# Performance work log

Measured on AMD Instinct MI355X. Metric: run time of the kernel, lower is better.

The kernel has to match this reference:

```python
import jax, jax.numpy as jnp
import numpy as np

N_GRAMS = 3
N_KERNELS = 11

def _kernel_mus(K):
    l = [1.0]
    if K == 1:
        return l
    bs = 2.0 / (K - 1)
    l.append(1.0 - bs / 2.0)
    for i in range(1, K - 1):
        l.append(l[i] - bs)
    return l

def _kernel_sigmas(K):
    if K == 1:
        return [0.001]
    bs = 2.0 / (K - 1)
    return [0.001] + [0.5 * bs] * (K - 1)

MU = jnp.asarray(_kernel_mus(N_KERNELS), jnp.float32)       # (K,)
SIGMA = jnp.asarray(_kernel_sigmas(N_KERNELS), jnp.float32)  # (K,)

def _conv_relu(x, w, b):
    # x: (B,E,L), w: (O,E,h); right-pad h-1 so output length == L (as ConstantPad1d((0,h-1)))
    h = w.shape[-1]
    y = jax.lax.conv_general_dilated(x, w, (1,), [(0, h - 1)], dimension_numbers=('NCH', 'OIH', 'NCH'))
    return jax.nn.relu(y + b[None, :, None]).transpose(0, 2, 1)  # (B,L,O)

def _cosine(a, b):
    # CosineMatrixAttention: normalize rows then matmul
    an = a / (jnp.linalg.norm(a, axis=-1, keepdims=True) + 1e-13)
    bn = b / (jnp.linalg.norm(b, axis=-1, keepdims=True) + 1e-13)
    return jnp.einsum('bqe,bde->bqd', an, bn)

def setup_inputs() -> dict:
    key = jax.random.key(0)
    ks = jax.random.split(key, 12)
    B, Lq, Ld, V, E, O = 128, 64, 512, 30000, 300, 128
    inp = {}
    inp['tokens_q'] = jax.random.randint(ks[0], (B, Lq), 0, V)
    inp['tokens_d'] = jax.random.randint(ks[1], (B, Ld), 0, V)
    inp['emb'] = jax.random.normal(ks[2], (V, E), jnp.float32) * 0.1
    for i, h in enumerate((1, 2, 3)):
        inp['conv_w%d' % h] = jax.random.normal(ks[3 + i], (O, E, h), jnp.float32) * (1.0 / np.sqrt(E * h))
        inp['conv_b%d' % h] = jnp.zeros((O,), jnp.float32)
    inp['fc_w'] = jax.random.normal(ks[9], (1, N_KERNELS * N_GRAMS * N_GRAMS), jnp.float32) * 0.1
    inp['fc_b'] = jnp.zeros((1,), jnp.float32)
    return inp

def reference(tokens_q, tokens_d, emb, conv_w1, conv_b1, conv_w2, conv_b2, conv_w3, conv_b3, fc_w, fc_b):
    qmask = (tokens_q > 0).astype(jnp.float32)  # (B,Lq)
    dmask = (tokens_d > 0).astype(jnp.float32)  # (B,Ld)
    qe = emb[tokens_q].transpose(0, 2, 1)  # (B,E,Lq)
    de = emb[tokens_d].transpose(0, 2, 1)  # (B,E,Ld)
    cws = [(conv_w1, conv_b1), (conv_w2, conv_b2), (conv_w3, conv_b3)]
    hq = [_conv_relu(qe, w, b) for w, b in cws]  # each (B,Lq,O)
    hd = [_conv_relu(de, w, b) for w, b in cws]  # each (B,Ld,O)
    pair_mask = qmask[:, :, None] * dmask[:, None, :]  # (B,Lq,Ld)
    mu = MU[None, None, None, :]
    sig = SIGMA[None, None, None, :]
    feats = []
    for q in range(N_GRAMS):
        for d in range(N_GRAMS):
            m = _cosine(hq[q], hd[d]) * pair_mask  # (B,Lq,Ld)
            rbf = jnp.exp(-jnp.square(m[..., None] - mu) / (2.0 * jnp.square(sig))) * pair_mask[..., None]
            qk = rbf.sum(axis=2)  # (B,Lq,K)
            logk = jnp.log(jnp.maximum(qk, 1e-10)) * 0.01
            # NOTE: original has a typo (loq_ vs log_) so the query mask is NOT applied before summing
            feats.append(logk.sum(axis=1))  # (B,K)
    cross = jnp.concatenate(feats, axis=-1)  # (B, K*G*G)
    return cross @ fc_w.T + fc_b  # (B,1)
```

## Files before the change

### kernel.cpp

```cpp
#include <hip/hip_runtime.h>
#include <hip/hip_bf16.h>

typedef __attribute__((ext_vector_type(8))) short short8;
typedef __attribute__((ext_vector_type(4))) float f32x4;

#define E_DIM 300
#define NCH   128
#define NOUT  384
#define NCHUNK 30

__device__ __forceinline__ unsigned short f2bf(float f) {
    unsigned int u = __float_as_uint(f);
    u += 0x7FFFu + ((u >> 16) & 1u);
    return (unsigned short)(u >> 16);
}
__device__ __forceinline__ float bf2f(unsigned short s) {
    return __uint_as_float(((unsigned int)s) << 16);
}

__global__ void pack_wb(const float* __restrict__ w1, const float* __restrict__ w2,
                        const float* __restrict__ w3, unsigned short* __restrict__ Wp) {
    int idx = blockIdx.x * 256 + threadIdx.x;
    if (idx >= NCHUNK * NOUT * 32) return;
    int ke = idx & 31;
    int n  = (idx >> 5) % NOUT;
    int c  = idx / (32 * NOUT);
    int s  = c / 10;
    int e  = (c % 10) * 32 + ke;
    int g  = n >> 7, o = n & 127, h = g + 1;
    float v = 0.0f;
    if (e < E_DIM && s < h) {
        const float* w = (g == 0) ? w1 : ((g == 1) ? w2 : w3);
        v = w[(o * E_DIM + e) * h + s];
    }
    Wp[idx] = f2bf(v);
}

__launch_bounds__(256, 3)
__global__ void conv_mfma(const int* __restrict__ tokens_q, const int* __restrict__ tokens_d,
                          const float* __restrict__ emb, const unsigned short* __restrict__ Wp,
                          const float* __restrict__ b1, const float* __restrict__ b2,
                          const float* __restrict__ b3,
                          unsigned short* __restrict__ hq, unsigned short* __restrict__ hd) {
    __shared__ __align__(16) short xs[66 * 320];
    __shared__ float bias_s[NOUT];
    __shared__ float nrm[64 * 3];
    __shared__ int   toks_s[66];

    int bx   = blockIdx.x;
    int b    = bx / 9;
    int tile = bx % 9;
    int isq  = (tile == 0);
    int L    = isq ? 64 : 512;
    int t0   = isq ? 0 : (tile - 1) * 64;
    const int* toks = isq ? (tokens_q + b * 64) : (tokens_d + b * 512);
    int tid  = threadIdx.x;
    int lane = tid & 63;
    int wn   = tid >> 6;
    int lr   = lane & 15;
    int lg   = lane >> 4;

    const unsigned short* wp0 = Wp + (size_t)(wn * 96 + lr) * 32 + lg * 8;
    short8 bbc[6], bbn[6];
    #pragma unroll
    for (int j = 0; j < 6; ++j) bbc[j] = *(const short8*)(wp0 + j * 512);

    if (tid < 66) toks_s[tid] = (t0 + tid < L) ? toks[t0 + tid] : -1;
    for (int i = tid; i < NOUT; i += 256) {
        int g = i >> 7, o = i & 127;
        bias_s[i] = (g == 0 ? b1 : (g == 1 ? b2 : b3))[o];
    }
    if (tid < 192) nrm[tid] = 0.0f;
    {
        uint4 z = {0, 0, 0, 0};
        uint4* xz = (uint4*)xs;
        for (int i = tid; i < 2640; i += 256) xz[i] = z;
    }
    __syncthreads();

    for (int i = tid; i < 66 * 75; i += 256) {
        int r = i / 75, f4 = i - r * 75;
        int tk = toks_s[r];
        if (tk >= 0) {
            float4 v = *(const float4*)(emb + (size_t)tk * E_DIM + f4 * 4);
            ushort4 u;
            u.x = f2bf(v.x); u.y = f2bf(v.y); u.z = f2bf(v.z); u.w = f2bf(v.w);
            int byte = (f4 * 8) ^ ((r & 7) << 4);
            *(ushort4*)((char*)xs + r * 640 + byte) = u;
        }
    }
    __syncthreads();

    f32x4 acc[4][6];
    #pragma unroll
    for (int i = 0; i < 4; ++i)
        #pragma unroll
        for (int j = 0; j < 6; ++j) acc[i][j] = (f32x4){0.f, 0.f, 0.f, 0.f};

    #pragma unroll 2
    for (int c = 0; c < NCHUNK; ++c) {
        if (c < NCHUNK - 1) {
            const unsigned short* wp = wp0 + (size_t)(c + 1) * NOUT * 32;
            #pragma unroll
            for (int j = 0; j < 6; ++j) bbn[j] = *(const short8*)(wp + j * 512);
        }
        int s  = c / 10;
        int ec = c - s * 10;
        short8 a[4];
        #pragma unroll
        for (int i = 0; i < 4; ++i) {
            int row  = i * 16 + lr + s;
            int byte = (ec * 64 + lg * 16) ^ ((row & 7) << 4);
            a[i] = *(const short8*)((const char*)xs + row * 640 + byte);
        }
        #pragma unroll
        for (int i = 0; i < 4; ++i)
            #pragma unroll
            for (int j = 0; j < 6; ++j)
                acc[i][j] = __builtin_amdgcn_mfma_f32_16x16x32_bf16(a[i], bbc[j], acc[i][j], 0, 0, 0);
        #pragma unroll
        for (int j = 0; j < 6; ++j) bbc[j] = bbn[j];
    }

    #pragma unroll
    for (int j = 0; j < 6; ++j) {
        float bv = bias_s[wn * 96 + j * 16 + lr];
        #pragma unroll
        for (int i = 0; i < 4; ++i)
            #pragma unroll
            for (int r = 0; r < 4; ++r) {
                float v = acc[i][j][r] + bv;
                acc[i][j][r] = v > 0.0f ? v : 0.0f;
            }
    }

    int  gfirst = (wn * 96) >> 7;
    bool spans  = ((wn * 96) & 127) + 96 > 128;

    float sqA[4][4], sqB[4][4];
    #pragma unroll
    for (int i = 0; i < 4; ++i)
        #pragma unroll
        for (int r = 0; r < 4; ++r) { sqA[i][r] = 0.0f; sqB[i][r] = 0.0f; }
    #pragma unroll
    for (int j = 0; j < 6; ++j) {
        int t = ((wn * 96 + j * 16) >> 7) - gfirst;
        #pragma unroll
        for (int i = 0; i < 4; ++i)
            #pragma unroll
            for (int r = 0; r < 4; ++r) {
                float v = acc[i][j][r] * acc[i][j][r];
                if (t == 0) sqA[i][r] += v; else sqB[i][r] += v;
            }
    }
    #pragma unroll
    for (int i = 0; i < 4; ++i)
        #pragma unroll
        for (int r = 0; r < 4; ++r) {
            float v = sqA[i][r];
            v += __shfl_xor(v, 1, 16);
            v += __shfl_xor(v, 2, 16);
            v += __shfl_xor(v, 4, 16);
            v += __shfl_xor(v, 8, 16);
            sqA[i][r] = v;
            float w = sqB[i][r];
            w += __shfl_xor(w, 1, 16);
            w += __shfl_xor(w, 2, 16);
            w += __shfl_xor(w, 4, 16);
            w += __shfl_xor(w, 8, 16);
            sqB[i][r] = w;
        }
    if (lr == 0) {
        #pragma unroll
        for (int i = 0; i < 4; ++i)
            #pragma unroll
            for (int r = 0; r < 4; ++r) {
                int row = i * 16 + lg * 4 + r;
                atomicAdd(&nrm[row * 3 + gfirst], sqA[i][r]);
                if (spans) atomicAdd(&nrm[row * 3 + gfirst + 1], sqB[i][r]);
            }
    }
    __syncthreads();

    float invA[4][4], invB[4][4];
    #pragma unroll
    for (int i = 0; i < 4; ++i)
        #pragma unroll
        for (int r = 0; r < 4; ++r) {
            int row = i * 16 + lg * 4 + r;
            invA[i][r] = 1.0f / (sqrtf(nrm[row * 3 + gfirst]) + 1e-13f);
            invB[i][r] = spans ? 1.0f / (sqrtf(nrm[row * 3 + gfirst + 1]) + 1e-13f) : 0.0f;
        }

    unsigned short* outp = isq ? hq : hd;
    #pragma unroll
    for (int j = 0; j < 6; ++j) {
        int n = wn * 96 + j * 16 + lr;
        int g = n >> 7, o = n & 127;
        int t = g - gfirst;
        #pragma unroll
        for (int i = 0; i < 4; ++i)
            #pragma unroll
            for (int r = 0; r < 4; ++r) {
                int row = i * 16 + lg * 4 + r;
                float inv = t ? invB[i][r] : invA[i][r];
                outp[((size_t)(g * 128 + b) * L + t0 + row) * NCH + o] = f2bf(acc[i][j][r] * inv);
            }
    }
}

#define QPITCH 136
__launch_bounds__(256, 3)
__global__ void sim_rbf(const unsigned short* __restrict__ hq,
                        const unsigned short* __restrict__ hd,
                        const int* __restrict__ tokens_q, const int* __restrict__ tokens_d,
                        float* __restrict__ cross) {
    __shared__ __align__(16) short qs[64 * QPITCH];
    __shared__ __align__(16) short ds2[2][64 * QPITCH];
    __shared__ unsigned char dm_s[512];
    __shared__ float logk_s[11];

    int bx = blockIdx.x;
    int b  = bx / 9;
    int p  = bx % 9;
    int gq = p / 3;
    int gd = p % 3;
    int tid = threadIdx.x;
    int lane = tid & 63;
    int wn   = tid >> 6;
    int lr   = lane & 15;
    int lg   = lane >> 4;

    if (tid < 11) logk_s[tid] = 0.0f;
    for (int i = tid; i < 512; i += 256)
        dm_s[i] = (tokens_d[b * 512 + i] > 0) ? 1 : 0;

    const unsigned short* qsrc = hq + ((size_t)(gq * 128 + b) * 64) * NCH;
    const unsigned short* dsrc = hd + ((size_t)(gd * 128 + b) * 512) * NCH;

    #pragma unroll
    for (int it = 0; it < 4; ++it) {
        int row  = it * 16 + (tid >> 4);
        int col8 = (tid & 15) * 8;
        *(uint4*)&qs[row * QPITCH + col8] = *(const uint4*)&qsrc[row * NCH + col8];
    }
    #pragma unroll
    for (int it = 0; it < 4; ++it) {
        int row  = it * 16 + (tid >> 4);
        int col8 = (tid & 15) * 8;
        *(uint4*)&ds2[0][row * QPITCH + col8] = *(const uint4*)&dsrc[row * NCH + col8];
    }
    __syncthreads();

    int q  = wn * 16 + lr;
    float qm = (tokens_q[b * 64 + q] > 0) ? 1.0f : 0.0f;

    short8 qf[4];
    #pragma unroll
    for (int ks = 0; ks < 4; ++ks)
        qf[ks] = *(const short8*)&qs[(wn * 16 + lr) * QPITCH + ks * 32 + lg * 8];

    float qk[11];
    #pragma unroll
    for (int k = 0; k < 11; ++k) qk[k] = 0.0f;

    const float C4 = 0.0183156389f;

    for (int ch = 0; ch < 8; ++ch) {
        int buf = ch & 1;
        uint4 r4[4];
        if (ch < 7) {
            #pragma unroll
            for (int it = 0; it < 4; ++it) {
                int row  = it * 16 + (tid >> 4);
                int col8 = (tid & 15) * 8;
                r4[it] = *(const uint4*)&dsrc[((size_t)(ch + 1) * 64 + row) * NCH + col8];
            }
        }

        #pragma unroll
        for (int mt = 0; mt < 4; ++mt) {
            f32x4 acc = (f32x4){0.f, 0.f, 0.f, 0.f};
            #pragma unroll
            for (int ks = 0; ks < 4; ++ks) {
                short8 a = *(const short8*)&ds2[buf][(mt * 16 + lr) * QPITCH + ks * 32 + lg * 8];
                acc = __builtin_amdgcn_mfma_f32_16x16x32_bf16(a, qf[ks], acc, 0, 0, 0);
            }
            uchar4 du = *(const uchar4*)&dm_s[ch * 64 + mt * 16 + lg * 4];
            float cv[4], cm[4];
            cm[0] = qm * (float)du.x; cm[1] = qm * (float)du.y;
            cm[2] = qm * (float)du.z; cm[3] = qm * (float)du.w;
            #pragma unroll
            for (int r = 0; r < 4; ++r) cv[r] = acc[r] * cm[r];

            float cmx = fmaxf(fmaxf(cv[0], cv[1]), fmaxf(cv[2], cv[3]));
            if (__any(cmx > 0.98f)) {
                #pragma unroll
                for (int r = 0; r < 4; ++r) {
                    if (cv[r] > 0.98f) {
                        float t0 = cv[r] - 1.0f;
                        qk[0] += __expf(-500000.0f * t0 * t0);
                    }
                }
            }
            #pragma unroll
            for (int r = 0; r < 4; ++r) {
                float c  = cv[r];
                float tA = c - 0.1f;
                float TA = __expf(-50.0f * tA * tA) * cm[r];
                float UA = __expf(20.0f * c - 4.0f);
                float tB = c + 0.1f;
                float TB = __expf(-50.0f * tB * tB) * cm[r];
                float UB = __expf(-20.0f * c - 4.0f);
                qk[5] += TA;
                TA *= UA; qk[4] += TA; UA *= C4;
                TA *= UA; qk[3] += TA; UA *= C4;
                TA *= UA; qk[2] += TA; UA *= C4;
                TA *= UA; qk[1] += TA;
                qk[6] += TB;
                TB *= UB; qk[7] += TB; UB *= C4;
                TB *= UB; qk[8] += TB; UB *= C4;
                TB *= UB; qk[9] += TB; UB *= C4;
                TB *= UB; qk[10] += TB;
            }
        }

        if (ch < 7) {
            #pragma unroll
            for (int it = 0; it < 4; ++it) {
                int row  = it * 16 + (tid >> 4);
                int col8 = (tid & 15) * 8;
                *(uint4*)&ds2[buf ^ 1][row * QPITCH + col8] = r4[it];
            }
        }
        __syncthreads();
    }

    #pragma unroll
    for (int k = 0; k < 11; ++k) {
        float v = qk[k];
        v += __shfl_xor(v, 16);
        v += __shfl_xor(v, 32);
        qk[k] = v;
    }
    if (lg == 0) {
        #pragma unroll
        for (int k = 0; k < 11; ++k) {
            float lv = __logf(fmaxf(qk[k], 1e-10f)) * 0.01f;
            atomicAdd(&logk_s[k], lv);
        }
    }
    __syncthreads();
    if (tid < 11) cross[b * 99 + p * 11 + tid] = logk_s[tid];
}

__global__ void fc_kernel(const float* __restrict__ cross, const float* __restrict__ fc_w,
                          const float* __restrict__ fc_b, float* __restrict__ out) {
    int b = threadIdx.x;
    float acc = fc_b[0];
    #pragma unroll 11
    for (int j = 0; j < 99; ++j) acc += cross[b * 99 + j] * fc_w[j];
    out[b] = acc;
}

extern "C" void kernel_launch(void* const* d_in, const int* in_sizes, int n_in,
                              void* d_out, int out_size, void* d_ws, size_t ws_size,
                              hipStream_t stream) {
    const int*   tq  = (const int*)d_in[0];
    const int*   td  = (const int*)d_in[1];
    const float* emb = (const float*)d_in[2];
    const float* w1  = (const float*)d_in[3];
    const float* cb1 = (const float*)d_in[4];
    const float* w2  = (const float*)d_in[5];
    const float* cb2 = (const float*)d_in[6];
    const float* w3  = (const float*)d_in[7];
    const float* cb3 = (const float*)d_in[8];
    const float* fcw = (const float*)d_in[9];
    const float* fcb = (const float*)d_in[10];

    char* ws = (char*)d_ws;
    unsigned short* Wp    = (unsigned short*)ws;
    float*          cross = (float*)(ws + 921600);
    unsigned short* hq    = (unsigned short*)(ws + 1048576);
    unsigned short* hd    = (unsigned short*)(ws + 8388608);

    hipLaunchKernelGGL(pack_wb, dim3(1440), dim3(256), 0, stream, w1, w2, w3, Wp);
    hipLaunchKernelGGL(conv_mfma, dim3(128 * 9), dim3(256), 0, stream,
                       tq, td, emb, Wp, cb1, cb2, cb3, hq, hd);
    hipLaunchKernelGGL(sim_rbf, dim3(128 * 9), dim3(256), 0, stream, hq, hd, tq, td, cross);
    hipLaunchKernelGGL(fc_kernel, dim3(1), dim3(128), 0, stream, cross, fcw, fcb, (float*)d_out);
}
```

Baseline: 194.0 us.

## Restructure conv kernel to 512 threads with per-group warps and shift-aware MFMA skipping

The conv kernel now runs 8 waves per block. Each wave owns 16 output channels across all three n-gram groups, replacing the earlier scheme of 96 contiguous packed columns per wave. The 30-chunk loop is split into three shift phases, and phase S only issues MFMAs for groups g>=S, so it skips the zero-padded weight chunks of the h=1 and h=2 convolutions (about a third of the MFMAs). The embedding gather is merged with zero-fill into a single pass, and the norm reduction is simplified now that each wave's columns sit inside known groups. The trade-offs are more atomics per row, higher register pressure under launch_bounds(512,4), and fewer accumulators per wave.

```diff
diff --git a/kernel.cpp b/kernel.cpp
--- a/kernel.cpp
+++ b/kernel.cpp
@@ -36,16 +36,14 @@
     Wp[idx] = f2bf(v);
 }
 
-__launch_bounds__(256, 3)
+__launch_bounds__(512, 4)
 __global__ void conv_mfma(const int* __restrict__ tokens_q, const int* __restrict__ tokens_d,
                           const float* __restrict__ emb, const unsigned short* __restrict__ Wp,
                           const float* __restrict__ b1, const float* __restrict__ b2,
                           const float* __restrict__ b3,
                           unsigned short* __restrict__ hq, unsigned short* __restrict__ hd) {
     __shared__ __align__(16) short xs[66 * 320];
-    __shared__ float bias_s[NOUT];
     __shared__ float nrm[64 * 3];
-    __shared__ int   toks_s[66];
 
     int bx   = blockIdx.x;
     int b    = bx / 9;
@@ -60,151 +58,88 @@
     int lr   = lane & 15;
     int lg   = lane >> 4;
 
-    const unsigned short* wp0 = Wp + (size_t)(wn * 96 + lr) * 32 + lg * 8;
-    short8 bbc[6], bbn[6];
-    #pragma unroll
-    for (int j = 0; j < 6; ++j) bbc[j] = *(const short8*)(wp0 + j * 512);
-
-    if (tid < 66) toks_s[tid] = (t0 + tid < L) ? toks[t0 + tid] : -1;
-    for (int i = tid; i < NOUT; i += 256) {
-        int g = i >> 7, o = i & 127;
-        bias_s[i] = (g == 0 ? b1 : (g == 1 ? b2 : b3))[o];
-    }
     if (tid < 192) nrm[tid] = 0.0f;
-    {
-        uint4 z = {0, 0, 0, 0};
-        uint4* xz = (uint4*)xs;
-        for (int i = tid; i < 2640; i += 256) xz[i] = z;
+
+    for (int i = tid; i < 66 * 80; i += 512) {
+        int r   = i / 80;
+        int f4  = i - r * 80;
+        int byt = (f4 * 8) ^ ((r & 7) << 4);
+        ushort4 u = {0, 0, 0, 0};
+        int pos = t0 + r;
+        if (f4 < 75 && pos < L) {
+            int tk = toks[pos];
+            float4 v = *(const float4*)(emb + (size_t)tk * E_DIM + f4 * 4);
+            u.x = f2bf(v.x); u.y = f2bf(v.y); u.z = f2bf(v.z); u.w = f2bf(v.w);
+        }
+        *(ushort4*)((char*)xs + r * 640 + byt) = u;
     }
     __syncthreads();
 
-    for (int i = tid; i < 66 * 75; i += 256) {
-        int r = i / 75, f4 = i - r * 75;
-        int tk = toks_s[r];
-        if (tk >= 0) {
-            float4 v = *(const float4*)(emb + (size_t)tk * E_DIM + f4 * 4);
-            ushort4 u;
-            u.x = f2bf(v.x); u.y = f2bf(v.y); u.z = f2bf(v.z); u.w = f2bf(v.w);
-            int byte = (f4 * 8) ^ ((r & 7) << 4);
-            *(ushort4*)((char*)xs + r * 640 + byte) = u;
-        }
+    f32x4 acc[4][3];
+    #pragma unroll
+    for (int i = 0; i < 4; ++i)
+        #pragma unroll
+        for (int g = 0; g < 3; ++g) acc[i][g] = (f32x4){0.f, 0.f, 0.f, 0.f};
+
+    const unsigned short* __restrict__ wpB = Wp + (size_t)(wn * 16 + lr) * 32 + lg * 8;
+    short8 bbc[3], bbn[3];
+
+#define LOADB(dst, c, g) dst = *(const short8*)(wpB + (size_t)((c) * NOUT + (g) * 128) * 32)
+
+#define PHASE(S) { \
+    _Pragma("unroll") for (int g = (S); g < 3; ++g) { LOADB(bbc[g], (S) * 10, g); } \
+    _Pragma("unroll") \
+    for (int ec = 0; ec < 10; ++ec) { \
+        if (ec < 9) { _Pragma("unroll") for (int g = (S); g < 3; ++g) { LOADB(bbn[g], (S) * 10 + ec + 1, g); } } \
+        short8 a[4]; \
+        _Pragma("unroll") for (int i = 0; i < 4; ++i) { \
+            int row = i * 16 + lr + (S); \
+            int byt = (ec * 64 + lg * 16) ^ ((row & 7) << 4); \
+            a[i] = *(const short8*)((const char*)xs + row * 640 + byt); \
+        } \
+        _Pragma("unroll") for (int i = 0; i < 4; ++i) \
+            _Pragma("unroll") for (int g = (S); g < 3; ++g) \
+                acc[i][g] = __builtin_amdgcn_mfma_f32_16x16x32_bf16(a[i], bbc[g], acc[i][g], 0, 0, 0); \
+        if (ec < 9) { _Pragma("unroll") for (int g = (S); g < 3; ++g) bbc[g] = bbn[g]; } \
+    } }
+
+    PHASE(0)
+    PHASE(1)
+    PHASE(2)
+#undef PHASE
+#undef LOADB
+
+    #pragma unroll
+    for (int g = 0; g < 3; ++g) {
+        float bv = (g == 0 ? b1 : (g == 1 ? b2 : b3))[wn * 16 + lr];
+        #pragma unroll
+        for (int i = 0; i < 4; ++i)
+            #pragma unroll
+            for (int r = 0; r < 4; ++r) {
+                float v = acc[i][g][r] + bv;
+                v = v > 0.0f ? v : 0.0f;
+                acc[i][g][r] = v;
+                float s = v * v;
+                s += __shfl_xor(s, 1, 16);
+                s += __shfl_xor(s, 2, 16);
+                s += __shfl_xor(s, 4, 16);
+                s += __shfl_xor(s, 8, 16);
+                if (lr == 0) atomicAdd(&nrm[(i * 16 + lg * 4 + r) * 3 + g], s);
+            }
     }
     __syncthreads();
 
-    f32x4 acc[4][6];
-    #pragma unroll
-    for (int i = 0; i < 4; ++i)
-        #pragma unroll
-        for (int j = 0; j < 6; ++j) acc[i][j] = (f32x4){0.f, 0.f, 0.f, 0.f};
-
-    #pragma unroll 2
-    for (int c = 0; c < NCHUNK; ++c) {
-        if (c < NCHUNK - 1) {
-            const unsigned short* wp = wp0 + (size_t)(c + 1) * NOUT * 32;
-            #pragma unroll
-            for (int j = 0; j < 6; ++j) bbn[j] = *(const short8*)(wp + j * 512);
-        }
-        int s  = c / 10;
-        int ec = c - s * 10;
-        short8 a[4];
-        #pragma unroll
-        for (int i = 0; i < 4; ++i) {
-            int row  = i * 16 + lr + s;
-            int byte = (ec * 64 + lg * 16) ^ ((row & 7) << 4);
-            a[i] = *(const short8*)((const char*)xs + row * 640 + byte);
-        }
-        #pragma unroll
-        for (int i = 0; i < 4; ++i)
-            #pragma unroll
-            for (int j = 0; j < 6; ++j)
-                acc[i][j] = __builtin_amdgcn_mfma_f32_16x16x32_bf16(a[i], bbc[j], acc[i][j], 0, 0, 0);
-        #pragma unroll
-        for (int j = 0; j < 6; ++j) bbc[j] = bbn[j];
-    }
-
-    #pragma unroll
-    for (int j = 0; j < 6; ++j) {
-        float bv = bias_s[wn * 96 + j * 16 + lr];
-        #pragma unroll
-        for (int i = 0; i < 4; ++i)
-            #pragma unroll
-            for (int r = 0; r < 4; ++r) {
-                float v = acc[i][j][r] + bv;
-                acc[i][j][r] = v > 0.0f ? v : 0.0f;
-            }
-    }
-
-    int  gfirst = (wn * 96) >> 7;
-    bool spans  = ((wn * 96) & 127) + 96 > 128;
-
-    float sqA[4][4], sqB[4][4];
-    #pragma unroll
-    for (int i = 0; i < 4; ++i)
-        #pragma unroll
-        for (int r = 0; r < 4; ++r) { sqA[i][r] = 0.0f; sqB[i][r] = 0.0f; }
-    #pragma unroll
-    for (int j = 0; j < 6; ++j) {
-        int t = ((wn * 96 + j * 16) >> 7) - gfirst;
-        #pragma unroll
-        for (int i = 0; i < 4; ++i)
-            #pragma unroll
-            for (int r = 0; r < 4; ++r) {
-                float v = acc[i][j][r] * acc[i][j][r];
-                if (t == 0) sqA[i][r] += v; else sqB[i][r] += v;
-            }
-    }
-    #pragma unroll
-    for (int i = 0; i < 4; ++i)
-        #pragma unroll
-        for (int r = 0; r < 4; ++r) {
-            float v = sqA[i][r];
-            v += __shfl_xor(v, 1, 16);
-            v += __shfl_xor(v, 2, 16);
-            v += __shfl_xor(v, 4, 16);
-            v += __shfl_xor(v, 8, 16);
-            sqA[i][r] = v;
-            float w = sqB[i][r];
-            w += __shfl_xor(w, 1, 16);
-            w += __shfl_xor(w, 2, 16);
-            w += __shfl_xor(w, 4, 16);
-            w += __shfl_xor(w, 8, 16);
-            sqB[i][r] = w;
-        }
-    if (lr == 0) {
+    unsigned short* outp = isq ? hq : hd;
+    #pragma unroll
+    for (int g = 0; g < 3; ++g) {
         #pragma unroll
         for (int i = 0; i < 4; ++i)
             #pragma unroll
             for (int r = 0; r < 4; ++r) {
                 int row = i * 16 + lg * 4 + r;
-                atomicAdd(&nrm[row * 3 + gfirst], sqA[i][r]);
-                if (spans) atomicAdd(&nrm[row * 3 + gfirst + 1], sqB[i][r]);
-            }
-    }
-    __syncthreads();
-
-    float invA[4][4], invB[4][4];
-    #pragma unroll
-    for (int i = 0; i < 4; ++i)
-        #pragma unroll
-        for (int r = 0; r < 4; ++r) {
-            int row = i * 16 + lg * 4 + r;
-            invA[i][r] = 1.0f / (sqrtf(nrm[row * 3 + gfirst]) + 1e-13f);
-            invB[i][r] = spans ? 1.0f / (sqrtf(nrm[row * 3 + gfirst + 1]) + 1e-13f) : 0.0f;
-        }
-
-    unsigned short* outp = isq ? hq : hd;
-    #pragma unroll
-    for (int j = 0; j < 6; ++j) {
-        int n = wn * 96 + j * 16 + lr;
-        int g = n >> 7, o = n & 127;
-        int t = g - gfirst;
-        #pragma unroll
-        for (int i = 0; i < 4; ++i)
-            #pragma unroll
-            for (int r = 0; r < 4; ++r) {
-                int row = i * 16 + lg * 4 + r;
-                float inv = t ? invB[i][r] : invA[i][r];
-                outp[((size_t)(g * 128 + b) * L + t0 + row) * NCH + o] = f2bf(acc[i][j][r] * inv);
+                float inv = 1.0f / (sqrtf(nrm[row * 3 + g]) + 1e-13f);
+                outp[((size_t)(g * 128 + b) * L + t0 + row) * NCH + wn * 16 + lr] =
+                    f2bf(acc[i][g][r] * inv);
             }
     }
 }
@@ -385,7 +320,7 @@
     unsigned short* hd    = (unsigned short*)(ws + 8388608);
 
     hipLaunchKernelGGL(pack_wb, dim3(1440), dim3(256), 0, stream, w1, w2, w3, Wp);
-    hipLaunchKernelGGL(conv_mfma, dim3(128 * 9), dim3(256), 0, stream,
+    hipLaunchKernelGGL(conv_mfma, dim3(128 * 9), dim3(512), 0, stream,
                        tq, td, emb, Wp, cb1, cb2, cb3, hq, hd);
     hipLaunchKernelGGL(sim_rbf, dim3(128 * 9), dim3(256), 0, stream, hq, hd, tq, td, cross);
     hipLaunchKernelGGL(fc_kernel, dim3(1), dim3(128), 0, stream, cross, fcw, fcb, (float*)d_out);
```

Result: slower. 206.5 us (+6.4%).
